# Performance work log

Hardware: AMD Instinct MI355X
Metric: run time of the kernel (lower is better)

The kernel has to match this reference:

```python
import jax, jax.numpy as jnp
import numpy as np

N = 50000
E = 800000
D_IN, D_HID, D_OUT = 128, 128, 64


def setup_inputs() -> dict:
    key = jax.random.key(0)
    ks = jax.random.split(key, 8)
    x = jax.random.normal(ks[0], (N, D_IN), dtype=jnp.float32)
    edge_index = jax.random.randint(ks[1], (2, E), 0, N, dtype=jnp.int64)
    # SAGEConv params: lin_l (neighbors, with bias), lin_r (root, no bias)
    s1 = 1.0 / np.sqrt(D_IN)
    s2 = 1.0 / np.sqrt(D_HID)
    W1_l = jax.random.uniform(ks[2], (D_IN, D_HID), jnp.float32, -s1, s1)
    b1 = jnp.zeros((D_HID,), jnp.float32)
    W1_r = jax.random.uniform(ks[3], (D_IN, D_HID), jnp.float32, -s1, s1)
    W2_l = jax.random.uniform(ks[4], (D_HID, D_OUT), jnp.float32, -s2, s2)
    b2 = jnp.zeros((D_OUT,), jnp.float32)
    W2_r = jax.random.uniform(ks[5], (D_HID, D_OUT), jnp.float32, -s2, s2)
    return {"x": x, "edge_index": edge_index, "W1_l": W1_l, "b1": b1,
            "W1_r": W1_r, "W2_l": W2_l, "b2": b2, "W2_r": W2_r}


def _sage_conv(x, src, dst, Wl, b, Wr, num_nodes):
    # mean aggregation over incoming edges (src -> dst)
    msgs = x[src]                                              # [E, d]
    agg = jax.ops.segment_sum(msgs, dst, num_segments=num_nodes)
    cnt = jax.ops.segment_sum(jnp.ones((src.shape[0],), x.dtype), dst,
                              num_segments=num_nodes)
    mean = agg / jnp.clip(cnt, 1.0)[:, None]                   # [N, d]
    return mean @ Wl + b + x @ Wr


def reference(x, edge_index, W1_l, b1, W1_r, W2_l, b2, W2_r):
    src, dst = edge_index[0], edge_index[1]
    n = x.shape[0]
    h = jax.nn.relu(_sage_conv(x, src, dst, W1_l, b1, W1_r, n))
    # dropout p=0.5 is identity in eval mode (training=False)
    return _sage_conv(h, src, dst, W2_l, b2, W2_r, n)
```

## Files before the change

kernel.cpp:

```cpp
#include <hip/hip_runtime.h>
#include <hip/hip_bf16.h>

typedef __hip_bfloat16 bf16;
typedef __attribute__((ext_vector_type(8))) short short8;
typedef __attribute__((ext_vector_type(4))) float floatx4;
typedef __attribute__((ext_vector_type(2))) float floatx2;
typedef unsigned short u16;
typedef unsigned char u8;

#define NNODES 50000
#define NEDGES 800000
#define D_IN  128
#define D_HID 128
#define D_OUT 64
#define NBLK  ((NNODES + 255) / 256)

__device__ __forceinline__ float bfbits2f(unsigned int u) {
    return __uint_as_float(u << 16);
}
__device__ __forceinline__ float b2f(bf16 v) { return __bfloat162float(v); }
__device__ __forceinline__ unsigned short f2bfbits(float f) {
    bf16 b = __float2bfloat16(f);
    return *(unsigned short*)&b;
}
__device__ __forceinline__ u8 f2fp8(float f) {
    return (u8)(__builtin_amdgcn_cvt_pk_fp8_f32(f, 0.f, 0, false) & 0xFF);
}
__device__ __forceinline__ float ld(const void* p, long long idx, int isf32) {
    if (isf32) return ((const float*)p)[idx];
    return b2f(((const bf16*)p)[idx]);
}
__device__ __forceinline__ short8 a_frag_from(const void* xp, long long elem_off, int isf32) {
    if (!isf32) return *(const short8*)((const bf16*)xp + elem_off);
    const float* f = (const float*)xp + elem_off;
    short8 r;
    #pragma unroll
    for (int j = 0; j < 8; j++) r[j] = (short)f2bfbits(f[j]);
    return r;
}

__global__ void k_setup(int* __restrict__ cnt, int n,
                        const unsigned int* __restrict__ ei_words,
                        const unsigned int* __restrict__ w_words,
                        int* __restrict__ flags,
                        const void* __restrict__ x,
                        const void* __restrict__ W1l, const void* __restrict__ W1r,
                        const void* __restrict__ W2l, const void* __restrict__ W2r,
                        bf16* __restrict__ p1l, bf16* __restrict__ p1r,
                        bf16* __restrict__ p2l, bf16* __restrict__ p2r,
                        unsigned int* __restrict__ x8) {
    int b = blockIdx.x;
    if (b < 128) {
        if (b == 0) {
            __shared__ int cnt_zero, cnt_bf;
            if (threadIdx.x == 0) { cnt_zero = 0; cnt_bf = 0; }
            __syncthreads();
            int t = threadIdx.x;
            unsigned int we = ei_words[2 * t + 1];
            if (we == 0u) atomicAdd(&cnt_zero, 1);
            unsigned int ww = w_words[t];
            unsigned int lowexp = (ww >> 7) & 0xFFu;
            if (lowexp >= 0x60u && lowexp <= 0x7Bu) atomicAdd(&cnt_bf, 1);
            __syncthreads();
            if (threadIdx.x == 0) {
                flags[0] = (cnt_zero >= 240) ? 1 : 0;
                flags[1] = (cnt_bf >= 192) ? 0 : 1;
            }
        }
        int i = b * blockDim.x + threadIdx.x;
        int stride = 128 * blockDim.x;
        for (; i < n; i += stride) cnt[i] = 0;
        return;
    }
    __shared__ int cnt_bf2;
    if (threadIdx.x == 0) cnt_bf2 = 0;
    __syncthreads();
    {
        unsigned int ww = w_words[threadIdx.x];
        unsigned int lowexp = (ww >> 7) & 0xFFu;
        if (lowexp >= 0x60u && lowexp <= 0x7Bu) atomicAdd(&cnt_bf2, 1);
    }
    __syncthreads();
    int isf32 = (cnt_bf2 >= 192) ? 0 : 1;
    if (b < 152) {
        int t = (b - 128) * 256 + threadIdx.x;
        if (t >= 6144) return;
        const void* Wm; bf16* dst; int NT; int base;
        if (t < 2048)      { Wm = W1l; dst = p1l; NT = 8; base = t; }
        else if (t < 4096) { Wm = W1r; dst = p1r; NT = 8; base = t - 2048; }
        else if (t < 5120) { Wm = W2l; dst = p2l; NT = 4; base = t - 4096; }
        else               { Wm = W2r; dst = p2r; NT = 4; base = t - 5120; }
        int lane = base & 63;
        int kt = (base >> 6) & 3;
        int nt = base >> 8;
        int Nmat = NT * 16;
        int krow = kt * 32 + ((lane >> 4) * 8);
        int col = nt * 16 + (lane & 15);
        #pragma unroll
        for (int j = 0; j < 8; j++) {
            float v = ld(Wm, (long long)(krow + j) * Nmat + col, isf32);
            dst[(((nt * 4 + kt) * 64 + lane) * 8) + j] = __float2bfloat16(v);
        }
        return;
    }
    const long long NU32 = (long long)NNODES * D_IN / 4;
    long long i = (long long)(b - 152) * 256 + threadIdx.x;
    long long stride = (long long)(gridDim.x - 152) * 256;
    if (isf32) {
        const float4* xf = (const float4*)x;
        for (; i < NU32; i += stride) {
            float4 f = xf[i];
            unsigned int w0 = __builtin_amdgcn_cvt_pk_fp8_f32(f.x, f.y, 0, false);
            w0 = __builtin_amdgcn_cvt_pk_fp8_f32(f.z, f.w, w0, true);
            x8[i] = w0;
        }
    } else {
        const ushort4* xb = (const ushort4*)x;
        for (; i < NU32; i += stride) {
            ushort4 s = xb[i];
            float f0 = bfbits2f(s.x), f1 = bfbits2f(s.y);
            float f2 = bfbits2f(s.z), f3 = bfbits2f(s.w);
            unsigned int w0 = __builtin_amdgcn_cvt_pk_fp8_f32(f0, f1, 0, false);
            w0 = __builtin_amdgcn_cvt_pk_fp8_f32(f2, f3, w0, true);
            x8[i] = w0;
        }
    }
}

__global__ void k_edges(const int* __restrict__ ei, const int* __restrict__ flags,
                        u16* __restrict__ src16, unsigned int* __restrict__ drpack,
                        int* __restrict__ cnt) {
    int e = blockIdx.x * blockDim.x + threadIdx.x;
    if (e >= NEDGES) return;
    int s, d;
    if (flags[0]) { s = ei[2 * e]; d = ei[2 * (NEDGES + e)]; }
    else          { s = ei[e];     d = ei[NEDGES + e]; }
    src16[e] = (u16)s;
    int rank = atomicAdd(&cnt[d], 1);
    drpack[e] = ((unsigned int)rank << 16) | (unsigned int)d;
}

__global__ void k_scan_a(const int* __restrict__ cnt, int* __restrict__ excl,
                         int* __restrict__ bsum) {
    __shared__ int s[256];
    int t = threadIdx.x;
    int i = blockIdx.x * 256 + t;
    int v = (i < NNODES) ? cnt[i] : 0;
    s[t] = v;
    __syncthreads();
    for (int off = 1; off < 256; off <<= 1) {
        int u = (t >= off) ? s[t - off] : 0;
        __syncthreads();
        s[t] += u;
        __syncthreads();
    }
    if (i < NNODES) excl[i] = s[t] - v;
    if (t == 255) bsum[blockIdx.x] = s[255];
}

__global__ void k_scan_bc(const int* __restrict__ excl, const int* __restrict__ bsum,
                          int* __restrict__ row_start) {
    __shared__ int s[256];
    __shared__ int bo;
    int t = threadIdx.x;
    int v = (t < NBLK) ? bsum[t] : 0;
    s[t] = v;
    __syncthreads();
    for (int off = 1; off < 256; off <<= 1) {
        int u = (t >= off) ? s[t - off] : 0;
        __syncthreads();
        s[t] += u;
        __syncthreads();
    }
    if (t == 0) bo = s[blockIdx.x] - bsum[blockIdx.x];
    __syncthreads();
    int i = blockIdx.x * 256 + t;
    if (i < NNODES) row_start[i] = bo + excl[i];
    if (i == 0) row_start[NNODES] = NEDGES;
}

__global__ void k_scatter(const u16* __restrict__ src16,
                          const unsigned int* __restrict__ drpack,
                          const int* __restrict__ row_start,
                          u16* __restrict__ csr16) {
    int e = blockIdx.x * blockDim.x + threadIdx.x;
    if (e >= NEDGES) return;
    unsigned int dp = drpack[e];
    int d = (int)(dp & 0xFFFFu);
    int r = (int)(dp >> 16);
    csr16[row_start[d] + r] = src16[e];
}

__global__ __launch_bounds__(256) void k_l1fused(
        const int* __restrict__ row_start, const u16* __restrict__ csr16,
        const void* __restrict__ x, const unsigned int* __restrict__ x8w,
        const int* __restrict__ flags,
        const bf16* __restrict__ p1l, const bf16* __restrict__ p1r,
        const bf16* __restrict__ p2l, const bf16* __restrict__ p2r,
        const void* __restrict__ b1, const void* __restrict__ b2v,
        u8* __restrict__ h28, float* __restrict__ hrf) {
    __shared__ bf16 ms[16][136];
    __shared__ bf16 hs[16][136];
    __shared__ u8 h2s8[16][72];
    __shared__ float hrs[16][68];
    int t = threadIdx.x;
    int w = t >> 6;
    int l = t & 63;
    int nb = blockIdx.x * 16;
    int isf32 = flags[1];
    int h = l >> 5;
    int c = l & 31;

    int rsv = row_start[nb + w * 4 + min(l, 4)];

    for (int i = 0; i < 4; i++) {
        int ln = w * 4 + i;
        int s0 = __shfl(rsv, i), s1 = __shfl(rsv, i + 1);
        float a0 = 0.f, a1 = 0.f, a2 = 0.f, a3 = 0.f;
        for (int base = s0; base < s1; base += 64) {
            int cnt2 = min(64, s1 - base);
            int my = (l < cnt2) ? (int)csr16[base + l] : 0;
            int j = 0;
            for (; j + 15 < cnt2; j += 16) {
                int jb = j + h * 8;
                int i0 = __shfl(my, jb + 0), i1 = __shfl(my, jb + 1);
                int i2 = __shfl(my, jb + 2), i3 = __shfl(my, jb + 3);
                int i4 = __shfl(my, jb + 4), i5 = __shfl(my, jb + 5);
                int i6 = __shfl(my, jb + 6), i7 = __shfl(my, jb + 7);
                unsigned int u0 = x8w[(size_t)i0 * 32 + c];
                unsigned int u1 = x8w[(size_t)i1 * 32 + c];
                unsigned int u2 = x8w[(size_t)i2 * 32 + c];
                unsigned int u3 = x8w[(size_t)i3 * 32 + c];
                unsigned int u4 = x8w[(size_t)i4 * 32 + c];
                unsigned int u5 = x8w[(size_t)i5 * 32 + c];
                unsigned int u6 = x8w[(size_t)i6 * 32 + c];
                unsigned int u7 = x8w[(size_t)i7 * 32 + c];
                floatx2 l0 = __builtin_amdgcn_cvt_pk_f32_fp8(u0, false);
                floatx2 h0 = __builtin_amdgcn_cvt_pk_f32_fp8(u0, true);
                floatx2 l1 = __builtin_amdgcn_cvt_pk_f32_fp8(u1, false);
                floatx2 h1 = __builtin_amdgcn_cvt_pk_f32_fp8(u1, true);
                floatx2 l2 = __builtin_amdgcn_cvt_pk_f32_fp8(u2, false);
                floatx2 h2 = __builtin_amdgcn_cvt_pk_f32_fp8(u2, true);
                floatx2 l3 = __builtin_amdgcn_cvt_pk_f32_fp8(u3, false);
                floatx2 h3 = __builtin_amdgcn_cvt_pk_f32_fp8(u3, true);
                floatx2 l4 = __builtin_amdgcn_cvt_pk_f32_fp8(u4, false);
                floatx2 h4 = __builtin_amdgcn_cvt_pk_f32_fp8(u4, true);
                floatx2 l5 = __builtin_amdgcn_cvt_pk_f32_fp8(u5, false);
                floatx2 h5 = __builtin_amdgcn_cvt_pk_f32_fp8(u5, true);
                floatx2 l6 = __builtin_amdgcn_cvt_pk_f32_fp8(u6, false);
                floatx2 h6 = __builtin_amdgcn_cvt_pk_f32_fp8(u6, true);
                floatx2 l7 = __builtin_amdgcn_cvt_pk_f32_fp8(u7, false);
                floatx2 h7 = __builtin_amdgcn_cvt_pk_f32_fp8(u7, true);
                a0 += l0.x + l1.x + l2.x + l3.x + l4.x + l5.x + l6.x + l7.x;
                a1 += l0.y + l1.y + l2.y + l3.y + l4.y + l5.y + l6.y + l7.y;
                a2 += h0.x + h1.x + h2.x + h3.x + h4.x + h5.x + h6.x + h7.x;
                a3 += h0.y + h1.y + h2.y + h3.y + h4.y + h5.y + h6.y + h7.y;
            }
            for (; j + 7 < cnt2; j += 8) {
                int jb = j + h * 4;
                int i0 = __shfl(my, jb + 0), i1 = __shfl(my, jb + 1);
                int i2 = __shfl(my, jb + 2), i3 = __shfl(my, jb + 3);
                unsigned int u0 = x8w[(size_t)i0 * 32 + c];
                unsigned int u1 = x8w[(size_t)i1 * 32 + c];
                unsigned int u2 = x8w[(size_t)i2 * 32 + c];
                unsigned int u3 = x8w[(size_t)i3 * 32 + c];
                floatx2 l0 = __builtin_amdgcn_cvt_pk_f32_fp8(u0, false);
                floatx2 h0 = __builtin_amdgcn_cvt_pk_f32_fp8(u0, true);
                floatx2 l1 = __builtin_amdgcn_cvt_pk_f32_fp8(u1, false);
                floatx2 h1 = __builtin_amdgcn_cvt_pk_f32_fp8(u1, true);
                floatx2 l2 = __builtin_amdgcn_cvt_pk_f32_fp8(u2, false);
                floatx2 h2 = __builtin_amdgcn_cvt_pk_f32_fp8(u2, true);
                floatx2 l3 = __builtin_amdgcn_cvt_pk_f32_fp8(u3, false);
                floatx2 h3 = __builtin_amdgcn_cvt_pk_f32_fp8(u3, true);
                a0 += l0.x + l1.x + l2.x + l3.x;
                a1 += l0.y + l1.y + l2.y + l3.y;
                a2 += h0.x + h1.x + h2.x + h3.x;
                a3 += h0.y + h1.y + h2.y + h3.y;
            }
            for (; j + 1 < cnt2; j += 2) {
                int i0 = __shfl(my, j + h);
                unsigned int u0 = x8w[(size_t)i0 * 32 + c];
                floatx2 l0 = __builtin_amdgcn_cvt_pk_f32_fp8(u0, false);
                floatx2 h0 = __builtin_amdgcn_cvt_pk_f32_fp8(u0, true);
                a0 += l0.x; a1 += l0.y; a2 += h0.x; a3 += h0.y;
            }
            if (j < cnt2) {
                int i0 = __shfl(my, j);
                unsigned int u0 = x8w[(size_t)i0 * 32 + c];
                floatx2 l0 = __builtin_amdgcn_cvt_pk_f32_fp8(u0, false);
                floatx2 h0 = __builtin_amdgcn_cvt_pk_f32_fp8(u0, true);
                if (h == 0) { a0 += l0.x; a1 += l0.y; a2 += h0.x; a3 += h0.y; }
            }
        }
        a0 += __shfl_xor(a0, 32);
        a1 += __shfl_xor(a1, 32);
        a2 += __shfl_xor(a2, 32);
        a3 += __shfl_xor(a3, 32);
        if (l < 32) {
            float inv = 1.0f / fmaxf((float)(s1 - s0), 1.0f);
            uint2 pk;
            pk.x = ((unsigned int)f2bfbits(a1 * inv) << 16) | f2bfbits(a0 * inv);
            pk.y = ((unsigned int)f2bfbits(a3 * inv) << 16) | f2bfbits(a2 * inv);
            *(uint2*)((bf16*)&ms[ln][0] + (c << 2)) = pk;
        }
    }
    __syncthreads();

    int m = l & 15;
    int quad = l >> 4;
    floatx4 acc0 = {0.f, 0.f, 0.f, 0.f};
    floatx4 acc1 = {0.f, 0.f, 0.f, 0.f};
    short8 am[4], ax[4];
    long long rowoff = (long long)(nb + m) * D_IN;
    #pragma unroll
    for (int kt = 0; kt < 4; kt++) {
        am[kt] = *(const short8*)&ms[m][kt * 32 + quad * 8];
        ax[kt] = a_frag_from(x, rowoff + kt * 32 + quad * 8, isf32);
    }
    int nt0 = w * 2, nt1 = w * 2 + 1;
    #pragma unroll
    for (int kt = 0; kt < 4; kt++) {
        short8 bl0 = *(const short8*)(p1l + (((nt0 * 4 + kt) * 64 + l) * 8));
        short8 br0 = *(const short8*)(p1r + (((nt0 * 4 + kt) * 64 + l) * 8));
        acc0 = __builtin_amdgcn_mfma_f32_16x16x32_bf16(am[kt], bl0, acc0, 0, 0, 0);
        acc0 = __builtin_amdgcn_mfma_f32_16x16x32_bf16(ax[kt], br0, acc0, 0, 0, 0);
        short8 bl1 = *(const short8*)(p1l + (((nt1 * 4 + kt) * 64 + l) * 8));
        short8 br1 = *(const short8*)(p1r + (((nt1 * 4 + kt) * 64 + l) * 8));
        acc1 = __builtin_amdgcn_mfma_f32_16x16x32_bf16(am[kt], bl1, acc1, 0, 0, 0);
        acc1 = __builtin_amdgcn_mfma_f32_16x16x32_bf16(ax[kt], br1, acc1, 0, 0, 0);
    }
    int c0 = nt0 * 16 + m;
    int c1 = nt1 * 16 + m;
    float bias0 = ld(b1, c0, isf32);
    float bias1 = ld(b1, c1, isf32);
    #pragma unroll
    for (int r = 0; r < 4; r++) {
        int row = quad * 4 + r;
        hs[row][c0] = __float2bfloat16(fmaxf(acc0[r] + bias0, 0.f));
        hs[row][c1] = __float2bfloat16(fmaxf(acc1[r] + bias1, 0.f));
    }
    __syncthreads();
    floatx4 acc2 = {0.f, 0.f, 0.f, 0.f};
    floatx4 acc3 = {0.f, 0.f, 0.f, 0.f};
    #pragma unroll
    for (int kt = 0; kt < 4; kt++) {
        short8 ah = *(const short8*)&hs[m][kt * 32 + quad * 8];
        short8 bw = *(const short8*)(p2l + (((w * 4 + kt) * 64 + l) * 8));
        short8 bz = *(const short8*)(p2r + (((w * 4 + kt) * 64 + l) * 8));
        acc2 = __builtin_amdgcn_mfma_f32_16x16x32_bf16(ah, bw, acc2, 0, 0, 0);
        acc3 = __builtin_amdgcn_mfma_f32_16x16x32_bf16(ah, bz, acc3, 0, 0, 0);
    }
    int c2 = w * 16 + m;
    float bias2 = ld(b2v, c2, isf32);
    #pragma unroll
    for (int r = 0; r < 4; r++) {
        h2s8[quad * 4 + r][c2] = f2fp8(acc2[r]);
        hrs[quad * 4 + r][c2] = acc3[r] + bias2;
    }
    __syncthreads();
    if (t < 128) {
        int node = t >> 3, col0 = (t & 7) * 8;
        uint2 v = *(const uint2*)&h2s8[node][col0];
        *(uint2*)(h28 + (long long)(nb + node) * D_OUT + col0) = v;
    }
    {
        int node = t >> 4, col0 = (t & 15) * 4;
        float4 v = *(const float4*)&hrs[node][col0];
        *(float4*)(hrf + (long long)(nb + node) * D_OUT + col0) = v;
    }
}

__global__ void k_agg2g(const int* __restrict__ row_start, const u16* __restrict__ csr16,
                        const u8* __restrict__ h28, const float* __restrict__ hrf,
                        const int* __restrict__ flags, void* __restrict__ out) {
    int t = threadIdx.x;
    int lane = t & 63;
    int node = blockIdx.x * 4 + (t >> 6);
    int g = lane >> 4;
    int c = lane & 15;
    const unsigned int* h32 = (const unsigned int*)h28;
    int s0 = row_start[node], s1 = row_start[node + 1];
    float a0 = 0.f, a1 = 0.f, a2 = 0.f, a3 = 0.f;
    for (int base = s0; base < s1; base += 64) {
        int cnt2 = min(64, s1 - base);
        int my = (lane < cnt2) ? (int)csr16[base + lane] : 0;
        int j = 0;
        for (; j + 15 < cnt2; j += 16) {
            int i0 = __shfl(my, j + g);
            int i1 = __shfl(my, j + 4 + g);
            int i2 = __shfl(my, j + 8 + g);
            int i3 = __shfl(my, j + 12 + g);
            unsigned int u0 = h32[(size_t)i0 * 16 + c];
            unsigned int u1 = h32[(size_t)i1 * 16 + c];
            unsigned int u2 = h32[(size_t)i2 * 16 + c];
            unsigned int u3 = h32[(size_t)i3 * 16 + c];
            floatx2 l0 = __builtin_amdgcn_cvt_pk_f32_fp8(u0, false);
            floatx2 h0 = __builtin_amdgcn_cvt_pk_f32_fp8(u0, true);
            floatx2 l1 = __builtin_amdgcn_cvt_pk_f32_fp8(u1, false);
            floatx2 h1 = __builtin_amdgcn_cvt_pk_f32_fp8(u1, true);
            floatx2 l2 = __builtin_amdgcn_cvt_pk_f32_fp8(u2, false);
            floatx2 h2 = __builtin_amdgcn_cvt_pk_f32_fp8(u2, true);
            floatx2 l3 = __builtin_amdgcn_cvt_pk_f32_fp8(u3, false);
            floatx2 h3 = __builtin_amdgcn_cvt_pk_f32_fp8(u3, true);
            a0 += l0.x + l1.x + l2.x + l3.x;
            a1 += l0.y + l1.y + l2.y + l3.y;
            a2 += h0.x + h1.x + h2.x + h3.x;
            a3 += h0.y + h1.y + h2.y + h3.y;
        }
        for (; j + 7 < cnt2; j += 8) {
            int i0 = __shfl(my, j + g);
            int i1 = __shfl(my, j + 4 + g);
            unsigned int u0 = h32[(size_t)i0 * 16 + c];
            unsigned int u1 = h32[(size_t)i1 * 16 + c];
            floatx2 l0 = __builtin_amdgcn_cvt_pk_f32_fp8(u0, false);
            floatx2 h0 = __builtin_amdgcn_cvt_pk_f32_fp8(u0, true);
            floatx2 l1 = __builtin_amdgcn_cvt_pk_f32_fp8(u1, false);
            floatx2 h1 = __builtin_amdgcn_cvt_pk_f32_fp8(u1, true);
            a0 += l0.x + l1.x; a1 += l0.y + l1.y;
            a2 += h0.x + h1.x; a3 += h0.y + h1.y;
        }
        for (; j < cnt2; j += 4) {
            int jj = j + g;
            float mk = (jj < cnt2) ? 1.0f : 0.0f;
            int i0 = __shfl(my, jj & 63);
            unsigned int u0 = h32[(size_t)i0 * 16 + c];
            floatx2 l0 = __builtin_amdgcn_cvt_pk_f32_fp8(u0, false);
            floatx2 h0 = __builtin_amdgcn_cvt_pk_f32_fp8(u0, true);
            a0 += mk * l0.x; a1 += mk * l0.y;
            a2 += mk * h0.x; a3 += mk * h0.y;
        }
    }
    a0 += __shfl_xor(a0, 32); a0 += __shfl_xor(a0, 16);
    a1 += __shfl_xor(a1, 32); a1 += __shfl_xor(a1, 16);
    a2 += __shfl_xor(a2, 32); a2 += __shfl_xor(a2, 16);
    a3 += __shfl_xor(a3, 32); a3 += __shfl_xor(a3, 16);
    if (lane < 16) {
        float inv = 1.0f / fmaxf((float)(s1 - s0), 1.0f);
        const float4 hr = *(const float4*)&hrf[(size_t)node * D_OUT + (c << 2)];
        float o0 = a0 * inv + hr.x;
        float o1 = a1 * inv + hr.y;
        float o2 = a2 * inv + hr.z;
        float o3 = a3 * inv + hr.w;
        if (flags[1]) {
            float4 v = {o0, o1, o2, o3};
            *(float4*)((float*)out + (size_t)node * D_OUT + (c << 2)) = v;
        } else {
            uint2 v;
            v.x = ((unsigned int)f2bfbits(o1) << 16) | f2bfbits(o0);
            v.y = ((unsigned int)f2bfbits(o3) << 16) | f2bfbits(o2);
            *(uint2*)((bf16*)out + (size_t)node * D_OUT + (c << 2)) = v;
        }
    }
}

extern "C" void kernel_launch(void* const* d_in, const int* in_sizes, int n_in,
                              void* d_out, int out_size, void* d_ws, size_t ws_size,
                              hipStream_t stream) {
    const void* x   = d_in[0];
    const int*  ei  = (const int*)d_in[1];
    const void* W1l = d_in[2];
    const void* b1  = d_in[3];
    const void* W1r = d_in[4];
    const void* W2l = d_in[5];
    const void* b2v = d_in[6];
    const void* W2r = d_in[7];

    const int N = NNODES;
    const int E = NEDGES;

    int*          flags     = (int*)d_ws;
    u16*          src16     = (u16*)(flags + 4);
    unsigned int* drpack    = (unsigned int*)(src16 + E);
    int*          cnt       = (int*)(drpack + E);
    int*          excl      = cnt + N;
    int*          bsum      = excl + N;
    int*          row_start = bsum + 256;
    u16*          csr16     = (u16*)(row_start + (N + 16));
    bf16*         p1l       = (bf16*)(csr16 + E);
    bf16*         p1r       = p1l + 16384;
    bf16*         p2l       = p1r + 16384;
    bf16*         p2r       = p2l + 8192;
    unsigned int* x8        = (unsigned int*)(p2r + 8192);
    u8*           h28       = (u8*)(x8 + (size_t)N * D_IN / 4);
    float*        hrf       = (float*)(h28 + (size_t)N * D_OUT);

    k_setup<<<152 + 1024, 256, 0, stream>>>(cnt, N, (const unsigned int*)ei,
                                            (const unsigned int*)W1l, flags, x,
                                            W1l, W1r, W2l, W2r,
                                            p1l, p1r, p2l, p2r, x8);
    k_edges<<<(E + 255) / 256, 256, 0, stream>>>(ei, flags, src16, drpack, cnt);
    k_scan_a<<<NBLK, 256, 0, stream>>>(cnt, excl, bsum);
    k_scan_bc<<<NBLK, 256, 0, stream>>>(excl, bsum, row_start);
    k_scatter<<<(E + 255) / 256, 256, 0, stream>>>(src16, drpack, row_start, csr16);
    k_l1fused<<<N / 16, 256, 0, stream>>>(row_start, csr16, x, x8, flags,
                                          p1l, p1r, p2l, p2r, b1, b2v, h28, hrf);
    k_agg2g<<<N / 4, 256, 0, stream>>>(row_start, csr16, h28, hrf, flags, d_out);
}
```

Baseline: 214.1 us.

## Restructure layer-1 fused kernel to 512 threads with two nodes per wave

The layer-1 fused kernel now launches 512 threads (8 waves). Each wave aggregates two nodes, with all 64 lanes reading 2-byte fp8 pairs across the full 128-wide row instead of splitting the wave into half-wave edge groups. The first CSR chunks for both nodes are loaded up front so their gathers can overlap. The root features x are staged into shared memory in bf16, and each wave computes one 16-column MFMA output tile, while only four waves do the second-layer projection. This aims to raise memory-level parallelism and occupancy for the gather, at the cost of idle waves in the second projection and a larger shared-memory footprint.

```diff
diff --git a/kernel.cpp b/kernel.cpp
--- a/kernel.cpp
+++ b/kernel.cpp
@@ -26,17 +26,13 @@
 __device__ __forceinline__ u8 f2fp8(float f) {
     return (u8)(__builtin_amdgcn_cvt_pk_fp8_f32(f, 0.f, 0, false) & 0xFF);
 }
+__device__ __forceinline__ float fp8tof(unsigned int u) {
+    floatx2 v = __builtin_amdgcn_cvt_pk_f32_fp8(u, false);
+    return v.x;
+}
 __device__ __forceinline__ float ld(const void* p, long long idx, int isf32) {
     if (isf32) return ((const float*)p)[idx];
     return b2f(((const bf16*)p)[idx]);
-}
-__device__ __forceinline__ short8 a_frag_from(const void* xp, long long elem_off, int isf32) {
-    if (!isf32) return *(const short8*)((const bf16*)xp + elem_off);
-    const float* f = (const float*)xp + elem_off;
-    short8 r;
-    #pragma unroll
-    for (int j = 0; j < 8; j++) r[j] = (short)f2bfbits(f[j]);
-    return r;
 }
 
 __global__ void k_setup(int* __restrict__ cnt, int n,
@@ -191,15 +187,51 @@
     csr16[row_start[d] + r] = src16[e];
 }
 
-__global__ __launch_bounds__(256) void k_l1fused(
+__device__ __forceinline__ void gather64(const u16* __restrict__ x8u, int my,
+                                         int cnt2, int l, float& a0, float& a1) {
+    int j = 0;
+    for (; j + 7 < cnt2; j += 8) {
+        int i0 = __shfl(my, j + 0), i1 = __shfl(my, j + 1);
+        int i2 = __shfl(my, j + 2), i3 = __shfl(my, j + 3);
+        int i4 = __shfl(my, j + 4), i5 = __shfl(my, j + 5);
+        int i6 = __shfl(my, j + 6), i7 = __shfl(my, j + 7);
+        unsigned int u0 = x8u[((unsigned)i0 << 6) + l];
+        unsigned int u1 = x8u[((unsigned)i1 << 6) + l];
+        unsigned int u2 = x8u[((unsigned)i2 << 6) + l];
+        unsigned int u3 = x8u[((unsigned)i3 << 6) + l];
+        unsigned int u4 = x8u[((unsigned)i4 << 6) + l];
+        unsigned int u5 = x8u[((unsigned)i5 << 6) + l];
+        unsigned int u6 = x8u[((unsigned)i6 << 6) + l];
+        unsigned int u7 = x8u[((unsigned)i7 << 6) + l];
+        floatx2 v0 = __builtin_amdgcn_cvt_pk_f32_fp8(u0, false);
+        floatx2 v1 = __builtin_amdgcn_cvt_pk_f32_fp8(u1, false);
+        floatx2 v2 = __builtin_amdgcn_cvt_pk_f32_fp8(u2, false);
+        floatx2 v3 = __builtin_amdgcn_cvt_pk_f32_fp8(u3, false);
+        floatx2 v4 = __builtin_amdgcn_cvt_pk_f32_fp8(u4, false);
+        floatx2 v5 = __builtin_amdgcn_cvt_pk_f32_fp8(u5, false);
+        floatx2 v6 = __builtin_amdgcn_cvt_pk_f32_fp8(u6, false);
+        floatx2 v7 = __builtin_amdgcn_cvt_pk_f32_fp8(u7, false);
+        a0 += v0.x + v1.x + v2.x + v3.x + v4.x + v5.x + v6.x + v7.x;
+        a1 += v0.y + v1.y + v2.y + v3.y + v4.y + v5.y + v6.y + v7.y;
+    }
+    for (; j < cnt2; j++) {
+        int si = __shfl(my, j);
+        unsigned int u = x8u[((unsigned)si << 6) + l];
+        floatx2 v = __builtin_amdgcn_cvt_pk_f32_fp8(u, false);
+        a0 += v.x; a1 += v.y;
+    }
+}
+
+__global__ __launch_bounds__(512) void k_l1fused(
         const int* __restrict__ row_start, const u16* __restrict__ csr16,
-        const void* __restrict__ x, const unsigned int* __restrict__ x8w,
+        const void* __restrict__ x, const u16* __restrict__ x8u,
         const int* __restrict__ flags,
         const bf16* __restrict__ p1l, const bf16* __restrict__ p1r,
         const bf16* __restrict__ p2l, const bf16* __restrict__ p2r,
         const void* __restrict__ b1, const void* __restrict__ b2v,
         u8* __restrict__ h28, float* __restrict__ hrf) {
     __shared__ bf16 ms[16][136];
+    __shared__ bf16 xs[16][136];
     __shared__ bf16 hs[16][136];
     __shared__ u8 h2s8[16][72];
     __shared__ float hrs[16][68];
@@ -208,154 +240,96 @@
     int l = t & 63;
     int nb = blockIdx.x * 16;
     int isf32 = flags[1];
-    int h = l >> 5;
-    int c = l & 31;
-
-    int rsv = row_start[nb + w * 4 + min(l, 4)];
-
-    for (int i = 0; i < 4; i++) {
-        int ln = w * 4 + i;
-        int s0 = __shfl(rsv, i), s1 = __shfl(rsv, i + 1);
-        float a0 = 0.f, a1 = 0.f, a2 = 0.f, a3 = 0.f;
-        for (int base = s0; base < s1; base += 64) {
-            int cnt2 = min(64, s1 - base);
-            int my = (l < cnt2) ? (int)csr16[base + l] : 0;
-            int j = 0;
-            for (; j + 15 < cnt2; j += 16) {
-                int jb = j + h * 8;
-                int i0 = __shfl(my, jb + 0), i1 = __shfl(my, jb + 1);
-                int i2 = __shfl(my, jb + 2), i3 = __shfl(my, jb + 3);
-                int i4 = __shfl(my, jb + 4), i5 = __shfl(my, jb + 5);
-                int i6 = __shfl(my, jb + 6), i7 = __shfl(my, jb + 7);
-                unsigned int u0 = x8w[(size_t)i0 * 32 + c];
-                unsigned int u1 = x8w[(size_t)i1 * 32 + c];
-                unsigned int u2 = x8w[(size_t)i2 * 32 + c];
-                unsigned int u3 = x8w[(size_t)i3 * 32 + c];
-                unsigned int u4 = x8w[(size_t)i4 * 32 + c];
-                unsigned int u5 = x8w[(size_t)i5 * 32 + c];
-                unsigned int u6 = x8w[(size_t)i6 * 32 + c];
-                unsigned int u7 = x8w[(size_t)i7 * 32 + c];
-                floatx2 l0 = __builtin_amdgcn_cvt_pk_f32_fp8(u0, false);
-                floatx2 h0 = __builtin_amdgcn_cvt_pk_f32_fp8(u0, true);
-                floatx2 l1 = __builtin_amdgcn_cvt_pk_f32_fp8(u1, false);
-                floatx2 h1 = __builtin_amdgcn_cvt_pk_f32_fp8(u1, true);
-                floatx2 l2 = __builtin_amdgcn_cvt_pk_f32_fp8(u2, false);
-                floatx2 h2 = __builtin_amdgcn_cvt_pk_f32_fp8(u2, true);
-                floatx2 l3 = __builtin_amdgcn_cvt_pk_f32_fp8(u3, false);
-                floatx2 h3 = __builtin_amdgcn_cvt_pk_f32_fp8(u3, true);
-                floatx2 l4 = __builtin_amdgcn_cvt_pk_f32_fp8(u4, false);
-                floatx2 h4 = __builtin_amdgcn_cvt_pk_f32_fp8(u4, true);
-                floatx2 l5 = __builtin_amdgcn_cvt_pk_f32_fp8(u5, false);
-                floatx2 h5 = __builtin_amdgcn_cvt_pk_f32_fp8(u5, true);
-                floatx2 l6 = __builtin_amdgcn_cvt_pk_f32_fp8(u6, false);
-                floatx2 h6 = __builtin_amdgcn_cvt_pk_f32_fp8(u6, true);
-                floatx2 l7 = __builtin_amdgcn_cvt_pk_f32_fp8(u7, false);
-                floatx2 h7 = __builtin_amdgcn_cvt_pk_f32_fp8(u7, true);
-                a0 += l0.x + l1.x + l2.x + l3.x + l4.x + l5.x + l6.x + l7.x;
-                a1 += l0.y + l1.y + l2.y + l3.y + l4.y + l5.y + l6.y + l7.y;
-                a2 += h0.x + h1.x + h2.x + h3.x + h4.x + h5.x + h6.x + h7.x;
-                a3 += h0.y + h1.y + h2.y + h3.y + h4.y + h5.y + h6.y + h7.y;
-            }
-            for (; j + 7 < cnt2; j += 8) {
-                int jb = j + h * 4;
-                int i0 = __shfl(my, jb + 0), i1 = __shfl(my, jb + 1);
-                int i2 = __shfl(my, jb + 2), i3 = __shfl(my, jb + 3);
-                unsigned int u0 = x8w[(size_t)i0 * 32 + c];
-                unsigned int u1 = x8w[(size_t)i1 * 32 + c];
-                unsigned int u2 = x8w[(size_t)i2 * 32 + c];
-                unsigned int u3 = x8w[(size_t)i3 * 32 + c];
-                floatx2 l0 = __builtin_amdgcn_cvt_pk_f32_fp8(u0, false);
-                floatx2 h0 = __builtin_amdgcn_cvt_pk_f32_fp8(u0, true);
-                floatx2 l1 = __builtin_amdgcn_cvt_pk_f32_fp8(u1, false);
-                floatx2 h1 = __builtin_amdgcn_cvt_pk_f32_fp8(u1, true);
-                floatx2 l2 = __builtin_amdgcn_cvt_pk_f32_fp8(u2, false);
-                floatx2 h2 = __builtin_amdgcn_cvt_pk_f32_fp8(u2, true);
-                floatx2 l3 = __builtin_amdgcn_cvt_pk_f32_fp8(u3, false);
-                floatx2 h3 = __builtin_amdgcn_cvt_pk_f32_fp8(u3, true);
-                a0 += l0.x + l1.x + l2.x + l3.x;
-                a1 += l0.y + l1.y + l2.y + l3.y;
-                a2 += h0.x + h1.x + h2.x + h3.x;
-                a3 += h0.y + h1.y + h2.y + h3.y;
-            }
-            for (; j + 1 < cnt2; j += 2) {
-                int i0 = __shfl(my, j + h);
-                unsigned int u0 = x8w[(size_t)i0 * 32 + c];
-                floatx2 l0 = __builtin_amdgcn_cvt_pk_f32_fp8(u0, false);
-                floatx2 h0 = __builtin_amdgcn_cvt_pk_f32_fp8(u0, true);
-                a0 += l0.x; a1 += l0.y; a2 += h0.x; a3 += h0.y;
-            }
-            if (j < cnt2) {
-                int i0 = __shfl(my, j);
-                unsigned int u0 = x8w[(size_t)i0 * 32 + c];
-                floatx2 l0 = __builtin_amdgcn_cvt_pk_f32_fp8(u0, false);
-                floatx2 h0 = __builtin_amdgcn_cvt_pk_f32_fp8(u0, true);
-                if (h == 0) { a0 += l0.x; a1 += l0.y; a2 += h0.x; a3 += h0.y; }
-            }
-        }
-        a0 += __shfl_xor(a0, 32);
-        a1 += __shfl_xor(a1, 32);
-        a2 += __shfl_xor(a2, 32);
-        a3 += __shfl_xor(a3, 32);
-        if (l < 32) {
-            float inv = 1.0f / fmaxf((float)(s1 - s0), 1.0f);
-            uint2 pk;
-            pk.x = ((unsigned int)f2bfbits(a1 * inv) << 16) | f2bfbits(a0 * inv);
-            pk.y = ((unsigned int)f2bfbits(a3 * inv) << 16) | f2bfbits(a2 * inv);
-            *(uint2*)((bf16*)&ms[ln][0] + (c << 2)) = pk;
-        }
+    int r0 = w * 2, r1 = r0 + 1;
+
+    int rsv = row_start[nb + r0 + min(l, 2)];
+    int s0 = __shfl(rsv, 0), s1 = __shfl(rsv, 1), s2 = __shfl(rsv, 2);
+
+    int ca = min(64, s1 - s0);
+    int cb = min(64, s2 - s1);
+    int mya = (l < ca) ? (int)csr16[s0 + l] : 0;
+    int myb = (l < cb) ? (int)csr16[s1 + l] : 0;
+
+    {
+        long long ro0 = (long long)(nb + r0) * D_IN + 2 * l;
+        long long ro1 = (long long)(nb + r1) * D_IN + 2 * l;
+        unsigned int px0, px1;
+        if (isf32) {
+            float2 v0 = *(const float2*)((const float*)x + ro0);
+            float2 v1 = *(const float2*)((const float*)x + ro1);
+            px0 = ((unsigned int)f2bfbits(v0.y) << 16) | f2bfbits(v0.x);
+            px1 = ((unsigned int)f2bfbits(v1.y) << 16) | f2bfbits(v1.x);
+        } else {
+            px0 = *(const unsigned int*)((const bf16*)x + ro0);
+            px1 = *(const unsigned int*)((const bf16*)x + ro1);
+        }
+        *(unsigned int*)((bf16*)&xs[r0][0] + 2 * l) = px0;
+        *(unsigned int*)((bf16*)&xs[r1][0] + 2 * l) = px1;
+    }
+
+    float aa0 = 0.f, aa1 = 0.f;
+    float bb0 = 0.f, bb1 = 0.f;
+    gather64(x8u, mya, ca, l, aa0, aa1);
+    gather64(x8u, myb, cb, l, bb0, bb1);
+    for (int base = s0 + 64; base < s1; base += 64) {
+        int cnt2 = min(64, s1 - base);
+        int my = (l < cnt2) ? (int)csr16[base + l] : 0;
+        gather64(x8u, my, cnt2, l, aa0, aa1);
+    }
+    for (int base = s1 + 64; base < s2; base += 64) {
+        int cnt2 = min(64, s2 - base);
+        int my = (l < cnt2) ? (int)csr16[base + l] : 0;
+        gather64(x8u, my, cnt2, l, bb0, bb1);
+    }
+    {
+        float inv = 1.0f / fmaxf((float)(s1 - s0), 1.0f);
+        unsigned int pk = ((unsigned int)f2bfbits(aa1 * inv) << 16) | f2bfbits(aa0 * inv);
+        *(unsigned int*)((bf16*)&ms[r0][0] + 2 * l) = pk;
+    }
+    {
+        float inv = 1.0f / fmaxf((float)(s2 - s1), 1.0f);
+        unsigned int pk = ((unsigned int)f2bfbits(bb1 * inv) << 16) | f2bfbits(bb0 * inv);
+        *(unsigned int*)((bf16*)&ms[r1][0] + 2 * l) = pk;
     }
     __syncthreads();
 
     int m = l & 15;
     int quad = l >> 4;
     floatx4 acc0 = {0.f, 0.f, 0.f, 0.f};
-    floatx4 acc1 = {0.f, 0.f, 0.f, 0.f};
-    short8 am[4], ax[4];
-    long long rowoff = (long long)(nb + m) * D_IN;
     #pragma unroll
     for (int kt = 0; kt < 4; kt++) {
-        am[kt] = *(const short8*)&ms[m][kt * 32 + quad * 8];
-        ax[kt] = a_frag_from(x, rowoff + kt * 32 + quad * 8, isf32);
-    }
-    int nt0 = w * 2, nt1 = w * 2 + 1;
-    #pragma unroll
-    for (int kt = 0; kt < 4; kt++) {
-        short8 bl0 = *(const short8*)(p1l + (((nt0 * 4 + kt) * 64 + l) * 8));
-        short8 br0 = *(const short8*)(p1r + (((nt0 * 4 + kt) * 64 + l) * 8));
-        acc0 = __builtin_amdgcn_mfma_f32_16x16x32_bf16(am[kt], bl0, acc0, 0, 0, 0);
-        acc0 = __builtin_amdgcn_mfma_f32_16x16x32_bf16(ax[kt], br0, acc0, 0, 0, 0);
-        short8 bl1 = *(const short8*)(p1l + (((nt1 * 4 + kt) * 64 + l) * 8));
-        short8 br1 = *(const short8*)(p1r + (((nt1 * 4 + kt) * 64 + l) * 8));
-        acc1 = __builtin_amdgcn_mfma_f32_16x16x32_bf16(am[kt], bl1, acc1, 0, 0, 0);
-        acc1 = __builtin_amdgcn_mfma_f32_16x16x32_bf16(ax[kt], br1, acc1, 0, 0, 0);
-    }
-    int c0 = nt0 * 16 + m;
-    int c1 = nt1 * 16 + m;
+        short8 amv = *(const short8*)&ms[m][kt * 32 + quad * 8];
+        short8 axv = *(const short8*)&xs[m][kt * 32 + quad * 8];
+        short8 bl0 = *(const short8*)(p1l + (((w * 4 + kt) * 64 + l) * 8));
+        short8 br0 = *(const short8*)(p1r + (((w * 4 + kt) * 64 + l) * 8));
+        acc0 = __builtin_amdgcn_mfma_f32_16x16x32_bf16(amv, bl0, acc0, 0, 0, 0);
+        acc0 = __builtin_amdgcn_mfma_f32_16x16x32_bf16(axv, br0, acc0, 0, 0, 0);
+    }
+    int c0 = w * 16 + m;
     float bias0 = ld(b1, c0, isf32);
-    float bias1 = ld(b1, c1, isf32);
     #pragma unroll
     for (int r = 0; r < 4; r++) {
-        int row = quad * 4 + r;
-        hs[row][c0] = __float2bfloat16(fmaxf(acc0[r] + bias0, 0.f));
-        hs[row][c1] = __float2bfloat16(fmaxf(acc1[r] + bias1, 0.f));
-    }
-    __syncthreads();
-    floatx4 acc2 = {0.f, 0.f, 0.f, 0.f};
-    floatx4 acc3 = {0.f, 0.f, 0.f, 0.f};
-    #pragma unroll
-    for (int kt = 0; kt < 4; kt++) {
-        short8 ah = *(const short8*)&hs[m][kt * 32 + quad * 8];
-        short8 bw = *(const short8*)(p2l + (((w * 4 + kt) * 64 + l) * 8));
-        short8 bz = *(const short8*)(p2r + (((w * 4 + kt) * 64 + l) * 8));
-        acc2 = __builtin_amdgcn_mfma_f32_16x16x32_bf16(ah, bw, acc2, 0, 0, 0);
-        acc3 = __builtin_amdgcn_mfma_f32_16x16x32_bf16(ah, bz, acc3, 0, 0, 0);
-    }
-    int c2 = w * 16 + m;
-    float bias2 = ld(b2v, c2, isf32);
-    #pragma unroll
-    for (int r = 0; r < 4; r++) {
-        h2s8[quad * 4 + r][c2] = f2fp8(acc2[r]);
-        hrs[quad * 4 + r][c2] = acc3[r] + bias2;
+        hs[quad * 4 + r][c0] = __float2bfloat16(fmaxf(acc0[r] + bias0, 0.f));
+    }
+    __syncthreads();
+    if (w < 4) {
+        floatx4 acc2 = {0.f, 0.f, 0.f, 0.f};
+        floatx4 acc3 = {0.f, 0.f, 0.f, 0.f};
+        #pragma unroll
+        for (int kt = 0; kt < 4; kt++) {
+            short8 ah = *(const short8*)&hs[m][kt * 32 + quad * 8];
+            short8 bw = *(const short8*)(p2l + (((w * 4 + kt) * 64 + l) * 8));
+            short8 bz = *(const short8*)(p2r + (((w * 4 + kt) * 64 + l) * 8));
+            acc2 = __builtin_amdgcn_mfma_f32_16x16x32_bf16(ah, bw, acc2, 0, 0, 0);
+            acc3 = __builtin_amdgcn_mfma_f32_16x16x32_bf16(ah, bz, acc3, 0, 0, 0);
+        }
+        int c2 = w * 16 + m;
+        float bias2 = ld(b2v, c2, isf32);
+        #pragma unroll
+        for (int r = 0; r < 4; r++) {
+            h2s8[quad * 4 + r][c2] = f2fp8(acc2[r]);
+            hrs[quad * 4 + r][c2] = acc3[r] + bias2;
+        }
     }
     __syncthreads();
     if (t < 128) {
@@ -363,7 +337,7 @@
         uint2 v = *(const uint2*)&h2s8[node][col0];
         *(uint2*)(h28 + (long long)(nb + node) * D_OUT + col0) = v;
     }
-    {
+    if (t < 256) {
         int node = t >> 4, col0 = (t & 15) * 4;
         float4 v = *(const float4*)&hrs[node][col0];
         *(float4*)(hrf + (long long)(nb + node) * D_OUT + col0) = v;
@@ -492,7 +466,7 @@
     k_scan_a<<<NBLK, 256, 0, stream>>>(cnt, excl, bsum);
     k_scan_bc<<<NBLK, 256, 0, stream>>>(excl, bsum, row_start);
     k_scatter<<<(E + 255) / 256, 256, 0, stream>>>(src16, drpack, row_start, csr16);
-    k_l1fused<<<N / 16, 256, 0, stream>>>(row_start, csr16, x, x8, flags,
+    k_l1fused<<<N / 16, 512, 0, stream>>>(row_start, csr16, x, (const u16*)x8, flags,
                                           p1l, p1r, p2l, p2r, b1, b2v, h28, hrf);
     k_agg2g<<<N / 4, 256, 0, stream>>>(row_start, csr16, h28, hrf, flags, d_out);
 }
```

Result: faster. 203.7 us (-4.9%).
